# Kernel optimization log

Hardware: AMD Instinct MI355X
Metric: run time of the kernel (lower is better)

Reference implementation:

```python
import jax, jax.numpy as jnp
import numpy as np

B, N, D = 2, 2048, 1024
H = 16                      # num_heads, head_dim = 64
E, K, CF = 4, 2, 1.0        # num_experts, top_k, capacity_factor
MLP_H = int(D * 4.0)        # dense Mlp hidden (mlp_ratio=4.0)
MOE_H = int(D * 0.25)       # expert hidden (hard-coded dim*0.25 in source)


def setup_inputs() -> dict:
    key = jax.random.key(0)
    ks = jax.random.split(key, 12)
    r = lambda k, shp, s=0.02: jax.random.normal(k, shp, jnp.float32) * s
    return dict(
        x=jax.random.normal(ks[0], (B, N, D), jnp.float32),
        noise=jax.random.normal(ks[1], (B, N, E), jnp.float32),
        ln1_g=jnp.ones((D,), jnp.float32), ln1_b=jnp.zeros((D,), jnp.float32),
        ln2_g=jnp.ones((D,), jnp.float32), ln2_b=jnp.zeros((D,), jnp.float32),
        w_qkv=r(ks[2], (3 * D, D)),
        w_proj=r(ks[3], (D, D)), b_proj=jnp.zeros((D,), jnp.float32),
        w_route=r(ks[4], (D, E), 0.05), b_route=jnp.zeros((E,), jnp.float32),
        w_noise=r(ks[5], (D, E), 0.05), b_noise=jnp.zeros((E,), jnp.float32),
        we1=r(ks[6], (E, D, MOE_H)), be1=jnp.zeros((E, MOE_H), jnp.float32),
        we2=r(ks[7], (E, MOE_H, D)), be2=jnp.zeros((E, D), jnp.float32),
        w_mlp1=r(ks[8], (D, MLP_H)), b_mlp1=jnp.zeros((MLP_H,), jnp.float32),
        w_mlp2=r(ks[9], (MLP_H, D)), b_mlp2=jnp.zeros((D,), jnp.float32),
    )


def _ln(x, g, b, eps=1e-5):
    mu = x.mean(-1, keepdims=True)
    var = ((x - mu) ** 2).mean(-1, keepdims=True)
    return (x - mu) * jax.lax.rsqrt(var + eps) * g + b


def _gelu(x):
    return jax.nn.gelu(x, approximate=False)  # torch nn.GELU default (erf)


def reference(x, noise, ln1_g, ln1_b, ln2_g, ln2_b, w_qkv, w_proj, b_proj,
              w_route, b_route, w_noise, b_noise, we1, be1, we2, be2,
              w_mlp1, b_mlp1, w_mlp2, b_mlp2):
    Bs, Ns, Ds = x.shape
    hd = Ds // H
    # --- attention branch ---
    x1 = _ln(x, ln1_g, ln1_b)
    qkv = (x1 @ w_qkv.T).reshape(Bs, Ns, 3, H, hd).transpose(2, 0, 3, 1, 4)
    q, k, v = qkv[0] * (hd ** -0.5), qkv[1], qkv[2]
    attn = jax.nn.softmax(jnp.einsum('bhnd,bhmd->bhnm', q, k), axis=-1)
    ao = jnp.einsum('bhnm,bhmd->bhnd', attn, v).transpose(0, 2, 1, 3).reshape(Bs, Ns, Ds)
    x = x + (ao @ w_proj.T + b_proj)
    # --- shared norm for mlp + moe ---
    x2 = _ln(x, ln2_g, ln2_b)
    # --- noisy top-k router ---
    logits = x2 @ w_route + b_route                  # [B,N,E]
    noisy = logits + noise * jax.nn.softplus(x2 @ w_noise + b_noise)
    topv, topi = jax.lax.top_k(noisy, K)             # [B,N,K]
    probs = jax.nn.softmax(topv, axis=-1)            # softmax over sparse logits == softmax over top-k
    T = Bs * Ns
    flat_x = x2.reshape(T, Ds)
    fidx = topi.reshape(T, K)
    rows = jnp.arange(T)[:, None]
    gate = jnp.zeros((T, E), noisy.dtype).at[rows, fidx].set(probs.reshape(T, K))
    capacity = int(T * K / E * CF)
    # --- capacity-limited dispatch / expert MLP / combine ---
    def dispatch(eid, W1, b1, W2, b2):
        mask = jnp.any(fidx == eid, axis=-1)                     # [T]
        order = jnp.argsort(jnp.logical_not(mask))               # stable: selected tokens first, in token order
        sel = order[:capacity]                                   # [C]
        valid = mask[sel].astype(flat_x.dtype)
        h = _gelu(flat_x[sel] @ W1 + b1)
        out = h @ W2 + b2
        w = gate[sel, eid] * valid
        return sel, out * w[:, None]
    sel, outw = jax.vmap(dispatch)(jnp.arange(E), we1, be1, we2, be2)   # [E,C], [E,C,D]
    moe = jnp.zeros_like(flat_x).at[sel.reshape(-1)].add(outw.reshape(-1, Ds)).reshape(Bs, Ns, Ds)
    # --- dense mlp branch ---
    mlp = _gelu(x2 @ w_mlp1 + b_mlp1) @ w_mlp2 + b_mlp2
    return x + mlp + moe
```

## Files before the change

### kernel.cpp

```cpp
#include <hip/hip_runtime.h>
#include <hip/hip_bf16.h>
#include <math.h>

typedef __bf16 bf16;
typedef __bf16 bf16x4 __attribute__((ext_vector_type(4)));
typedef __bf16 bf16x8 __attribute__((ext_vector_type(8)));
typedef float  f32x4  __attribute__((ext_vector_type(4)));

#define T_TOK 4096
#define DIM   1024
#define NHEAD 16
#define SEQ   2048
#define NEXP  4
#define CAP   2048
#define MLPH  4096
#define MOEH  256

__device__ __forceinline__ float gelu_exact(float v) {
    return 0.5f * v * (1.f + erff(v * 0.70710678118654752f));
}

struct HL { bf16 h, l; };
__device__ __forceinline__ HL split2(float v) {
    HL r; r.h = (bf16)v; r.l = (bf16)(v - (float)r.h); return r;
}

__device__ __forceinline__ float fast_exp2(float x) {
#if __has_builtin(__builtin_amdgcn_exp2f)
    return __builtin_amdgcn_exp2f(x);
#else
    return exp2f(x);
#endif
}

__device__ __forceinline__ void gload16(const bf16* gptr, bf16* lptr) {
    __builtin_amdgcn_global_load_lds(
        (const __attribute__((address_space(1))) unsigned int*)gptr,
        (__attribute__((address_space(3))) unsigned int*)lptr,
        16, 0, 0);
}

__device__ __forceinline__ bf16x8 sw_frag(const bf16* arr, int row, int cc) {
    return *(const bf16x8*)&arr[row * 64 + ((cc ^ (row & 7)) * 8)];
}

__device__ __forceinline__ void xcd_tile(int& bx, int& by) {
    int gx = gridDim.x;
    int nwg = gx * gridDim.y;
    int flat = blockIdx.y * gx + blockIdx.x;
    int q = nwg >> 3, r = nwg & 7;
    int xcd = flat & 7, loc = flat >> 3;
    int swz = (xcd < r ? xcd * (q + 1) : r * (q + 1) + (xcd - r) * q) + loc;
    bx = swz % gx; by = swz / gx;
}

__global__ __launch_bounds__(256)
void ln_split_kernel(const float* __restrict__ x, const float* __restrict__ g,
                     const float* __restrict__ b, bf16* __restrict__ oh, bf16* __restrict__ ol) {
    int wave = threadIdx.x >> 6, lane = threadIdx.x & 63;
    long t = (long)blockIdx.x * 4 + wave;
    const float* xr = x + t * DIM;
    float v[16];
    #pragma unroll
    for (int i = 0; i < 16; i++) v[i] = xr[i * 64 + lane];
    float s = 0.f, s2 = 0.f;
    #pragma unroll
    for (int i = 0; i < 16; i++) { s += v[i]; s2 += v[i] * v[i]; }
    #pragma unroll
    for (int m = 1; m < 64; m <<= 1) { s += __shfl_xor(s, m); s2 += __shfl_xor(s2, m); }
    float mu  = s * (1.f / DIM);
    float var = s2 * (1.f / DIM) - mu * mu;
    float rs  = 1.f / sqrtf(var + 1e-5f);
    #pragma unroll
    for (int i = 0; i < 16; i++) {
        int d = i * 64 + lane;
        HL sp = split2((v[i] - mu) * rs * g[d] + b[d]);
        oh[t * DIM + d] = sp.h; ol[t * DIM + d] = sp.l;
    }
}

__global__ __launch_bounds__(256)
void split_pair_kernel(const float* __restrict__ in, bf16* __restrict__ h, bf16* __restrict__ l) {
    long i0 = ((long)blockIdx.x * 256 + threadIdx.x) * 4;
    f32x4 v = *(const f32x4*)&in[i0];
    bf16x4 vh, vl;
    #pragma unroll
    for (int j = 0; j < 4; j++) { HL sp = split2(v[j]); vh[j] = sp.h; vl[j] = sp.l; }
    *(bf16x4*)&h[i0] = vh; *(bf16x4*)&l[i0] = vl;
}

__global__ __launch_bounds__(256)
void transpose_conv_kernel(const float* __restrict__ in, bf16* __restrict__ out, int R, int C) {
    __shared__ bf16 tile[32][33];
    long bo = (long)blockIdx.z * R * C;
    in += bo; out += bo;
    int c0 = blockIdx.x * 32, r0 = blockIdx.y * 32;
    int tx = threadIdx.x & 31, ty = threadIdx.x >> 5;
    #pragma unroll
    for (int i = 0; i < 32; i += 8)
        tile[ty + i][tx] = (bf16)in[(long)(r0 + ty + i) * C + c0 + tx];
    __syncthreads();
    #pragma unroll
    for (int i = 0; i < 32; i += 8)
        out[(long)(c0 + ty + i) * R + r0 + tx] = tile[tx][ty + i];
}

__global__ __launch_bounds__(256)
void gemm_qkv(const bf16* __restrict__ Ah_g, const bf16* __restrict__ Al_g,
              const bf16* __restrict__ Bh_g, const bf16* __restrict__ Bl_g,
              bf16* __restrict__ Qh_g, bf16* __restrict__ Ql_g,
              bf16* __restrict__ Kh_g, bf16* __restrict__ Kl_g,
              bf16* __restrict__ VtI) {
    const int K = DIM;
    __shared__ alignas(16) bf16 Ah[8192], Al[8192], Bh[8192], Bl[8192];
    int tid = threadIdx.x;
    int wave = tid >> 6, lane = tid & 63;
    int l16 = lane & 15, l4 = lane >> 4;
    int wr = (wave >> 1) * 64, wc = (wave & 1) * 64;
    int bx, by; xcd_tile(bx, by);
    int row0 = by * 128, col0 = bx * 128;
    int r8s = lane >> 3;
    int colb = ((lane & 7) ^ r8s) * 8;
    f32x4 acc[4][4] = {};
    for (int k0 = 0; k0 < K; k0 += 64) {
        #pragma unroll
        for (int p = 0; p < 4; p++) {
            int rl = p * 32 + wave * 8 + r8s;
            int lb = p * 2048 + wave * 512;
            gload16(&Ah_g[(long)(row0 + rl) * K + k0 + colb], &Ah[lb]);
            gload16(&Al_g[(long)(row0 + rl) * K + k0 + colb], &Al[lb]);
            gload16(&Bh_g[(long)(col0 + rl) * K + k0 + colb], &Bh[lb]);
            gload16(&Bl_g[(long)(col0 + rl) * K + k0 + colb], &Bl[lb]);
        }
        __syncthreads();
        #pragma unroll
        for (int ks = 0; ks < 2; ks++) {
            bf16x8 ah[4], al[4], bh[4], bl[4];
            #pragma unroll
            for (int i = 0; i < 4; i++) {
                ah[i] = sw_frag(Ah, wr + i*16 + l16, ks*4 + l4);
                al[i] = sw_frag(Al, wr + i*16 + l16, ks*4 + l4);
            }
            #pragma unroll
            for (int j = 0; j < 4; j++) {
                bh[j] = sw_frag(Bh, wc + j*16 + l16, ks*4 + l4);
                bl[j] = sw_frag(Bl, wc + j*16 + l16, ks*4 + l4);
            }
            #pragma unroll
            for (int i = 0; i < 4; i++)
                #pragma unroll
                for (int j = 0; j < 4; j++) {
                    acc[i][j] = __builtin_amdgcn_mfma_f32_16x16x32_bf16(ah[i], bh[j], acc[i][j], 0, 0, 0);
                    acc[i][j] = __builtin_amdgcn_mfma_f32_16x16x32_bf16(ah[i], bl[j], acc[i][j], 0, 0, 0);
                    acc[i][j] = __builtin_amdgcn_mfma_f32_16x16x32_bf16(al[i], bh[j], acc[i][j], 0, 0, 0);
                }
        }
        __syncthreads();
    }
    if (col0 < 2048) {
        bool isQ = (col0 < 1024);
        bf16* oh = isQ ? Qh_g : Kh_g;
        bf16* ol = isQ ? Ql_g : Kl_g;
        float qscale = isQ ? 0.18033688011112043f : 1.0f;
        #pragma unroll
        for (int i = 0; i < 4; i++)
            #pragma unroll
            for (int r = 0; r < 4; r++) {
                int t = row0 + wr + i * 16 + l4 * 4 + r;
                int bq = t >> 11, s = t & 2047;
                #pragma unroll
                for (int j = 0; j < 4; j++) {
                    int col = (col0 + wc + j * 16 + l16) & 1023;
                    int hh = col >> 6, dl = col & 63;
                    long o = ((long)(bq * NHEAD + hh) * SEQ + s) * 64 + dl;
                    HL sp = split2(acc[i][j][r] * qscale);
                    oh[o] = sp.h;
                    if (!isQ) ol[o] = sp.l;
                }
            }
    } else {
        #pragma unroll
        for (int i = 0; i < 4; i++) {
            int s0 = row0 + wr + i * 16 + l4 * 4;
            int b = s0 >> 11, sl = s0 & 2047;
            #pragma unroll
            for (int j = 0; j < 4; j++) {
                int d = col0 - 2048 + wc + j * 16 + l16;
                int h = d >> 6, dl = d & 63;
                long base = ((long)(b * NHEAD + h) * 64 + dl) * (2 * SEQ) + 2 * sl;
                bf16x8 vi;
                #pragma unroll
                for (int r = 0; r < 4; r++) {
                    HL sp = split2(acc[i][j][r]);
                    vi[2 * r] = sp.h; vi[2 * r + 1] = sp.l;
                }
                *(bf16x8*)&VtI[base] = vi;
            }
        }
    }
}

__global__ __launch_bounds__(512, 4)
void flash_attn(const bf16* __restrict__ Qh_g,
                const bf16* __restrict__ Kh_g, const bf16* __restrict__ Kl_g,
                const bf16* __restrict__ VtI_g,
                bf16* __restrict__ aoh, bf16* __restrict__ aol) {
    __shared__ alignas(16) bf16 KhS[2][4096], KlS[2][4096], VIS[2][8192];
    int tid = threadIdx.x;
    int wave = tid >> 6, lane = tid & 63;
    int l16 = lane & 15, l4 = lane >> 4;
    int bid = blockIdx.x;
    int bh = bid & 31;
    int b = bh >> 4, h = bh & 15;
    int q0 = (bid >> 5) * 128;

    bf16x8 qfh[2];
    {
        const bf16* qh = Qh_g + ((long)bh * SEQ + q0 + wave * 16 + l16) * 64;
        #pragma unroll
        for (int ks = 0; ks < 2; ks++)
            qfh[ks] = *(const bf16x8*)&qh[ks * 32 + l4 * 8];
    }
    int r8 = lane >> 3;
    int c8 = lane & 7;
    int r4 = lane >> 4, c16 = lane & 15;
    const bf16* kh_g = Kh_g + (long)bh * SEQ * 64;
    const bf16* kl_g = Kl_g + (long)bh * SEQ * 64;
    const bf16* vI_g = VtI_g + (long)bh * 64 * (2 * SEQ);

    float m_s = -1e30f, l_s = 0.f;
    f32x4 accO[4] = {};

    auto stage = [&](int c0, int bsel) {
        int R0 = wave * 8;
        int row = R0 + r8;
        int ksw = (c8 ^ r8) * 8;
        gload16(&kh_g[(long)(c0 + row) * 64 + ksw], &KhS[bsel][R0 * 64]);
        gload16(&kl_g[(long)(c0 + row) * 64 + ksw], &KlS[bsel][R0 * 64]);
        #pragma unroll
        for (int q = 0; q < 2; q++) {
            int d0 = R0 + q * 4 + r4;
            gload16(&vI_g[(long)d0 * (2 * SEQ) + 2 * c0 + ((c16 ^ (d0 & 15)) * 8)],
                    &VIS[bsel][(R0 + q * 4) * 128]);
        }
    };

    auto compute = [&](const bf16* KhT, const bf16* KlT, const bf16* VIT) {
        f32x4 st[4] = {};
        __builtin_amdgcn_s_setprio(1);
        #pragma unroll
        for (int ks = 0; ks < 2; ks++) {
            #pragma unroll
            for (int i = 0; i < 4; i++) {
                bf16x8 akh = sw_frag(KhT, i * 16 + l16, ks * 4 + l4);
                bf16x8 akl = sw_frag(KlT, i * 16 + l16, ks * 4 + l4);
                st[i] = __builtin_amdgcn_mfma_f32_16x16x32_bf16(akh, qfh[ks], st[i], 0, 0, 0);
                st[i] = __builtin_amdgcn_mfma_f32_16x16x32_bf16(akl, qfh[ks], st[i], 0, 0, 0);
            }
        }
        __builtin_amdgcn_s_setprio(0);
        float mx = st[0][0];
        #pragma unroll
        for (int i = 0; i < 4; i++)
            #pragma unroll
            for (int r = 0; r < 4; r++) mx = fmaxf(mx, st[i][r]);
        mx = fmaxf(mx, __shfl_xor(mx, 16));
        mx = fmaxf(mx, __shfl_xor(mx, 32));
        if (!__all(mx <= m_s + 8.f)) {
            float mnew = fmaxf(m_s, mx);
            float alpha = fast_exp2(m_s - mnew);
            l_s *= alpha;
            #pragma unroll
            for (int i = 0; i < 4; i++)
                #pragma unroll
                for (int r = 0; r < 4; r++) accO[i][r] *= alpha;
            m_s = mnew;
        }
        float psum = 0.f;
        bf16x8 pw[4];
        #pragma unroll
        for (int kb = 0; kb < 4; kb++)
            #pragma unroll
            for (int r = 0; r < 4; r++) {
                float pv = fast_exp2(st[kb][r] - m_s);
                psum += pv;
                bf16 pb = (bf16)pv;
                pw[kb][2 * r] = pb; pw[kb][2 * r + 1] = pb;
            }
        psum += __shfl_xor(psum, 16);
        psum += __shfl_xor(psum, 32);
        l_s += psum;
        __builtin_amdgcn_s_setprio(1);
        #pragma unroll
        for (int kb = 0; kb < 4; kb++) {
            #pragma unroll
            for (int i = 0; i < 4; i++) {
                int d = i * 16 + l16;
                bf16x8 av = *(const bf16x8*)&VIT[d * 128 + (((kb * 4 + l4) ^ (d & 15)) * 8)];
                accO[i] = __builtin_amdgcn_mfma_f32_16x16x32_bf16(av, pw[kb], accO[i], 0, 0, 0);
            }
        }
        __builtin_amdgcn_s_setprio(0);
    };

    const int NT = SEQ / 64;
    stage(0, 0);
    #pragma unroll 1
    for (int t = 0; t < NT; t += 2) {
        stage((t + 1) * 64, 1);
        asm volatile("s_waitcnt vmcnt(4)" ::: "memory");
        __builtin_amdgcn_sched_barrier(0);
        __builtin_amdgcn_s_barrier();
        compute(KhS[0], KlS[0], VIS[0]);
        asm volatile("" ::: "memory");
        __builtin_amdgcn_s_barrier();
        if (t + 2 < NT) {
            stage((t + 2) * 64, 0);
            asm volatile("s_waitcnt vmcnt(4)" ::: "memory");
        } else {
            asm volatile("s_waitcnt vmcnt(0)" ::: "memory");
        }
        __builtin_amdgcn_sched_barrier(0);
        __builtin_amdgcn_s_barrier();
        compute(KhS[1], KlS[1], VIS[1]);
        asm volatile("" ::: "memory");
        __builtin_amdgcn_s_barrier();
    }

    float inv = 1.f / l_s;
    int q = q0 + wave * 16 + l16;
    #pragma unroll
    for (int i = 0; i < 4; i++) {
        bf16x4 oh4, ol4;
        #pragma unroll
        for (int r = 0; r < 4; r++) { HL sp = split2(accO[i][r] * inv); oh4[r] = sp.h; ol4[r] = sp.l; }
        long o = ((long)(b * SEQ + q)) * DIM + h * 64 + i * 16 + l4 * 4;
        *(bf16x4*)&aoh[o] = oh4;
        *(bf16x4*)&aol[o] = ol4;
    }
}

__global__ __launch_bounds__(256)
void gemm_proj(const bf16* __restrict__ Ah_g, const bf16* __restrict__ Al_g,
               const bf16* __restrict__ Bh_g, const bf16* __restrict__ Bl_g,
               const float* __restrict__ bias, const float* __restrict__ res,
               float* __restrict__ C, int N, int K) {
    __shared__ alignas(16) bf16 Ah[8192], Al[8192], Bh[8192], Bl[8192];
    int tid = threadIdx.x;
    int wave = tid >> 6, lane = tid & 63;
    int l16 = lane & 15, l4 = lane >> 4;
    int wr = (wave >> 1) * 64, wc = (wave & 1) * 64;
    int bx, by; xcd_tile(bx, by);
    int row0 = by * 128, col0 = bx * 128;
    int r8s = lane >> 3;
    int colb = ((lane & 7) ^ r8s) * 8;
    f32x4 acc[4][4] = {};
    for (int k0 = 0; k0 < K; k0 += 64) {
        #pragma unroll
        for (int p = 0; p < 4; p++) {
            int rl = p * 32 + wave * 8 + r8s;
            int lb = p * 2048 + wave * 512;
            gload16(&Ah_g[(long)(row0 + rl) * K + k0 + colb], &Ah[lb]);
            gload16(&Al_g[(long)(row0 + rl) * K + k0 + colb], &Al[lb]);
            gload16(&Bh_g[(long)(col0 + rl) * K + k0 + colb], &Bh[lb]);
            gload16(&Bl_g[(long)(col0 + rl) * K + k0 + colb], &Bl[lb]);
        }
        __syncthreads();
        #pragma unroll
        for (int ks = 0; ks < 2; ks++) {
            bf16x8 ah[4], al[4], bh[4], bl[4];
            #pragma unroll
            for (int i = 0; i < 4; i++) {
                ah[i] = sw_frag(Ah, wr + i*16 + l16, ks*4 + l4);
                al[i] = sw_frag(Al, wr + i*16 + l16, ks*4 + l4);
            }
            #pragma unroll
            for (int j = 0; j < 4; j++) {
                bh[j] = sw_frag(Bh, wc + j*16 + l16, ks*4 + l4);
                bl[j] = sw_frag(Bl, wc + j*16 + l16, ks*4 + l4);
            }
            #pragma unroll
            for (int i = 0; i < 4; i++)
                #pragma unroll
                for (int j = 0; j < 4; j++) {
                    acc[i][j] = __builtin_amdgcn_mfma_f32_16x16x32_bf16(ah[i], bh[j], acc[i][j], 0, 0, 0);
                    acc[i][j] = __builtin_amdgcn_mfma_f32_16x16x32_bf16(ah[i], bl[j], acc[i][j], 0, 0, 0);
                    acc[i][j] = __builtin_amdgcn_mfma_f32_16x16x32_bf16(al[i], bh[j], acc[i][j], 0, 0, 0);
                }
        }
        __syncthreads();
    }
    #pragma unroll
    for (int i = 0; i < 4; i++)
        #pragma unroll
        for (int r = 0; r < 4; r++) {
            int grow = row0 + wr + i * 16 + l4 * 4 + r;
            #pragma unroll
            for (int j = 0; j < 4; j++) {
                int gcol = col0 + wc + j * 16 + l16;
                long o = (long)grow * N + gcol;
                C[o] = acc[i][j][r] + bias[gcol] + res[o];
            }
        }
}

template<bool BIAS, bool GELU, bool GATHER, int OUT_MODE>
__global__ __launch_bounds__(256)
void gemm_bt(const bf16* __restrict__ A, const bf16* __restrict__ Bt,
             const float* __restrict__ bias,
             bf16* __restrict__ Cbf, float* __restrict__ Cf,
             const int* __restrict__ rowmap, const float* __restrict__ roww,
             int M, int N, int K,
             long eA, long eB, long ebias, long eMap, long eC) {
    int ez = blockIdx.z;
    A += (long)ez * eA; Bt += (long)ez * eB;
    if (BIAS) bias += (long)ez * ebias;
    if (GATHER || OUT_MODE == 3) rowmap += (long)ez * eMap;
    if (OUT_MODE == 3) roww += (long)ez * eMap;
    if (OUT_MODE == 0) Cbf += (long)ez * eC;

    __shared__ alignas(16) bf16 As[8192];
    __shared__ alignas(16) bf16 Bs[8192];
    int tid = threadIdx.x;
    int wave = tid >> 6, lane = tid & 63;
    int l16 = lane & 15, l4 = lane >> 4;
    int wr = (wave >> 1) * 64, wc = (wave & 1) * 64;
    int bx, by; xcd_tile(bx, by);
    int row0 = by * 128, col0 = bx * 128;
    int r8s = lane >> 3;
    int colb = ((lane & 7) ^ r8s) * 8;

    long arow[4];
    #pragma unroll
    for (int p = 0; p < 4; p++) {
        long gr = row0 + p * 32 + wave * 8 + r8s;
        if (GATHER) gr = rowmap[gr];
        arow[p] = gr;
    }
    f32x4 acc[4][4] = {};
    for (int k0 = 0; k0 < K; k0 += 64) {
        #pragma unroll
        for (int p = 0; p < 4; p++) {
            int rl = p * 32 + wave * 8 + r8s;
            int lb = p * 2048 + wave * 512;
            gload16(&A[arow[p] * K + k0 + colb], &As[lb]);
            gload16(&Bt[(long)(col0 + rl) * K + k0 + colb], &Bs[lb]);
        }
        __syncthreads();
        #pragma unroll
        for (int ks = 0; ks < 2; ks++) {
            bf16x8 af[4], bfr[4];
            #pragma unroll
            for (int i = 0; i < 4; i++) af[i]  = sw_frag(As, wr + i*16 + l16, ks*4 + l4);
            #pragma unroll
            for (int j = 0; j < 4; j++) bfr[j] = sw_frag(Bs, wc + j*16 + l16, ks*4 + l4);
            #pragma unroll
            for (int i = 0; i < 4; i++)
                #pragma unroll
                for (int j = 0; j < 4; j++)
                    acc[i][j] = __builtin_amdgcn_mfma_f32_16x16x32_bf16(af[i], bfr[j], acc[i][j], 0, 0, 0);
        }
        __syncthreads();
    }
    #pragma unroll
    for (int i = 0; i < 4; i++)
        #pragma unroll
        for (int r = 0; r < 4; r++) {
            int grow = row0 + wr + i * 16 + l4 * 4 + r;
            int st = 0; float sw = 0.f;
            if (OUT_MODE == 3) { st = rowmap[grow]; sw = roww[grow]; }
            #pragma unroll
            for (int j = 0; j < 4; j++) {
                int gcol = col0 + wc + j * 16 + l16;
                float v = acc[i][j][r];
                if (BIAS) v += bias[gcol];
                if (GELU) v = gelu_exact(v);
                if (OUT_MODE == 0) {
                    Cbf[(long)grow * N + gcol] = (bf16)v;
                } else if (OUT_MODE == 2) {
                    long o = (long)grow * N + gcol;
                    Cf[o] += v;
                } else {
                    atomicAdd(&Cf[(long)st * N + gcol], sw * v);
                }
            }
        }
}

__global__ __launch_bounds__(256)
void routing_kernel(const float* __restrict__ xres, const float* __restrict__ g,
                    const float* __restrict__ b, const float* __restrict__ w_route,
                    const float* __restrict__ b_route, const float* __restrict__ w_noise,
                    const float* __restrict__ b_noise, const float* __restrict__ noise,
                    int* __restrict__ topi, float* __restrict__ topp,
                    bf16* __restrict__ x2b) {
    int wave = threadIdx.x >> 6, lane = threadIdx.x & 63;
    long t = (long)blockIdx.x * 4 + wave;
    const float* xr = xres + t * DIM;
    float v[16];
    #pragma unroll
    for (int i = 0; i < 16; i++) v[i] = xr[i * 64 + lane];
    float s = 0.f, s2 = 0.f;
    #pragma unroll
    for (int i = 0; i < 16; i++) { s += v[i]; s2 += v[i] * v[i]; }
    #pragma unroll
    for (int m = 1; m < 64; m <<= 1) { s += __shfl_xor(s, m); s2 += __shfl_xor(s2, m); }
    float mu  = s * (1.f / DIM);
    float var = s2 * (1.f / DIM) - mu * mu;
    float rs  = 1.f / sqrtf(var + 1e-5f);
    float accr[4] = {0.f,0.f,0.f,0.f}, accn[4] = {0.f,0.f,0.f,0.f};
    #pragma unroll
    for (int i = 0; i < 16; i++) {
        int d = i * 64 + lane;
        float n = (v[i] - mu) * rs * g[d] + b[d];
        x2b[t * DIM + d] = (bf16)n;
        #pragma unroll
        for (int e = 0; e < 4; e++) {
            accr[e] += n * w_route[d * 4 + e];
            accn[e] += n * w_noise[d * 4 + e];
        }
    }
    #pragma unroll
    for (int e = 0; e < 4; e++)
        #pragma unroll
        for (int m = 1; m < 64; m <<= 1) {
            accr[e] += __shfl_xor(accr[e], m);
            accn[e] += __shfl_xor(accn[e], m);
        }
    if (lane == 0) {
        float nz[4];
        #pragma unroll
        for (int e = 0; e < 4; e++) {
            float logit = accr[e] + b_route[e];
            float si = accn[e] + b_noise[e];
            float sp = si > 0.f ? si + log1pf(expf(-si)) : log1pf(expf(si));
            nz[e] = logit + noise[t * 4 + e] * sp;
        }
        int i1 = 0;
        #pragma unroll
        for (int e = 1; e < 4; e++) if (nz[e] > nz[i1]) i1 = e;
        int i2 = -1; float v2 = -1e30f;
        #pragma unroll
        for (int e = 0; e < 4; e++) if (e != i1 && nz[e] > v2) { v2 = nz[e]; i2 = e; }
        float ex = expf(v2 - nz[i1]);
        topi[t * 2]     = i1; topi[t * 2 + 1] = i2;
        topp[t * 2]     = 1.f / (1.f + ex);
        topp[t * 2 + 1] = ex / (1.f + ex);
    }
}

__global__ __launch_bounds__(256)
void dispatch_kernel(const int* __restrict__ topi, const float* __restrict__ topp,
                     int* __restrict__ sel, float* __restrict__ wgt) {
    int e = threadIdx.x >> 6, lane = threadIdx.x & 63;
    int cnt = 0;
    for (int c = 0; c < T_TOK; c += 64) {
        int t = c + lane;
        int i0 = topi[t * 2], i1 = topi[t * 2 + 1];
        bool m = (i0 == e) || (i1 == e);
        unsigned long long bal = __ballot(m);
        int pos = cnt + __popcll(bal & ((1ull << lane) - 1ull));
        if (m && pos < CAP) {
            sel[e * CAP + pos] = t;
            wgt[e * CAP + pos] = (i0 == e) ? topp[t * 2] : topp[t * 2 + 1];
        }
        cnt += (int)__popcll(bal);
    }
    if (cnt > CAP) cnt = CAP;
    for (int pos = cnt + lane; pos < CAP; pos += 64) {
        sel[e * CAP + pos] = 0;
        wgt[e * CAP + pos] = 0.f;
    }
}

extern "C" void kernel_launch(void* const* d_in, const int* in_sizes, int n_in,
                              void* d_out, int out_size, void* d_ws, size_t ws_size,
                              hipStream_t stream) {
    (void)in_sizes; (void)n_in; (void)out_size; (void)ws_size;
    const float* x       = (const float*)d_in[0];
    const float* noise   = (const float*)d_in[1];
    const float* ln1_g   = (const float*)d_in[2];
    const float* ln1_b   = (const float*)d_in[3];
    const float* ln2_g   = (const float*)d_in[4];
    const float* ln2_b   = (const float*)d_in[5];
    const float* w_qkv   = (const float*)d_in[6];
    const float* w_proj  = (const float*)d_in[7];
    const float* b_proj  = (const float*)d_in[8];
    const float* w_route = (const float*)d_in[9];
    const float* b_route = (const float*)d_in[10];
    const float* w_noise = (const float*)d_in[11];
    const float* b_noise = (const float*)d_in[12];
    const float* we1     = (const float*)d_in[13];
    const float* be1     = (const float*)d_in[14];
    const float* we2     = (const float*)d_in[15];
    const float* be2     = (const float*)d_in[16];
    const float* w_mlp1  = (const float*)d_in[17];
    const float* b_mlp1  = (const float*)d_in[18];
    const float* w_mlp2  = (const float*)d_in[19];
    const float* b_mlp2  = (const float*)d_in[20];
    float* d_outf = (float*)d_out;

    const size_t MB = 1024 * 1024;
    char* ws = (char*)d_ws;
    bf16* x1h = (bf16*)(ws);
    bf16* x1l = (bf16*)(ws + 8 * MB);
    bf16* aoh = (bf16*)(ws);
    bf16* aol = (bf16*)(ws + 8 * MB);
    bf16* w_mlp1T = (bf16*)(ws);
    bf16* w_mlp2T = (bf16*)(ws + 8 * MB);
    bf16* wqkvh = (bf16*)(ws + 16 * MB);
    bf16* wqkvl = (bf16*)(ws + 22 * MB);
    bf16* we1T  = (bf16*)(ws + 16 * MB);
    bf16* we2T  = (bf16*)(ws + 18 * MB);
    bf16* h_e   = (bf16*)(ws + 20 * MB);
    bf16* wprojh = (bf16*)(ws + 28 * MB);
    bf16* wprojl = (bf16*)(ws + 30 * MB);
    bf16* Qh = (bf16*)(ws + 32 * MB);
    bf16* Ql = (bf16*)(ws + 40 * MB);
    bf16* Kh = (bf16*)(ws + 48 * MB);
    bf16* Kl = (bf16*)(ws + 56 * MB);
    bf16* h_mlp = (bf16*)(ws + 32 * MB);
    bf16*  VtI  = (bf16*)(ws + 64 * MB);
    bf16*  x2b  = (bf16*)(ws + 64 * MB);
    int*   topi = (int*)(ws + 72 * MB);
    float* topp = (float*)(ws + 72 * MB + 32768);
    int*   sel  = (int*)(ws + 72 * MB + 65536);
    float* wgt  = (float*)(ws + 72 * MB + 98304);

    ln_split_kernel<<<T_TOK/4, 256, 0, stream>>>(x, ln1_g, ln1_b, x1h, x1l);
    split_pair_kernel<<<(3*DIM*DIM)/1024, 256, 0, stream>>>(w_qkv, wqkvh, wqkvl);
    split_pair_kernel<<<(DIM*DIM)/1024,   256, 0, stream>>>(w_proj, wprojh, wprojl);

    gemm_qkv<<<dim3(3*DIM/128, T_TOK/128), 256, 0, stream>>>(
        x1h, x1l, wqkvh, wqkvl, Qh, Ql, Kh, Kl, VtI);

    flash_attn<<<dim3(32 * (SEQ/128)), 512, 0, stream>>>(Qh, Kh, Kl, VtI, aoh, aol);

    gemm_proj<<<dim3(DIM/128, T_TOK/128), 256, 0, stream>>>(
        aoh, aol, wprojh, wprojl, b_proj, x, d_outf, DIM, DIM);

    routing_kernel<<<T_TOK/4, 256, 0, stream>>>(d_outf, ln2_g, ln2_b, w_route, b_route,
                                                w_noise, b_noise, noise, topi, topp, x2b);
    dispatch_kernel<<<1, 256, 0, stream>>>(topi, topp, sel, wgt);

    transpose_conv_kernel<<<dim3(MLPH/32, DIM/32, 1),    256, 0, stream>>>(w_mlp1, w_mlp1T, DIM, MLPH);
    transpose_conv_kernel<<<dim3(DIM/32, MLPH/32, 1),    256, 0, stream>>>(w_mlp2, w_mlp2T, MLPH, DIM);
    transpose_conv_kernel<<<dim3(MOEH/32, DIM/32, NEXP), 256, 0, stream>>>(we1, we1T, DIM, MOEH);
    transpose_conv_kernel<<<dim3(DIM/32, MOEH/32, NEXP), 256, 0, stream>>>(we2, we2T, MOEH, DIM);

    gemm_bt<true,true,false,0><<<dim3(MLPH/128, T_TOK/128), 256, 0, stream>>>(
        x2b, w_mlp1T, b_mlp1, h_mlp, nullptr, nullptr, nullptr, T_TOK, MLPH, DIM,
        0, 0, 0, 0, 0);
    gemm_bt<true,false,false,2><<<dim3(DIM/128, T_TOK/128), 256, 0, stream>>>(
        h_mlp, w_mlp2T, b_mlp2, nullptr, d_outf, nullptr, nullptr, T_TOK, DIM, MLPH,
        0, 0, 0, 0, 0);

    gemm_bt<true,true,true,0><<<dim3(MOEH/128, CAP/128, NEXP), 256, 0, stream>>>(
        x2b, we1T, be1, h_e, nullptr, sel, nullptr, CAP, MOEH, DIM,
        0, (long)MOEH*DIM, MOEH, CAP, (long)CAP*MOEH);
    gemm_bt<true,false,false,3><<<dim3(DIM/128, CAP/128, NEXP), 256, 0, stream>>>(
        h_e, we2T, be2, nullptr, d_outf, sel, wgt, CAP, DIM, MOEH,
        (long)CAP*MOEH, (long)DIM*MOEH, DIM, CAP, 0);
}
```

Measured before the change: 626.4 us.

## Double-buffer GEMM LDS tiles with BK=32 and overlap global loads with MFMA

The three GEMM kernels now use a two-stage LDS ping-pong with K-tile 32, issuing the next tile's global_load_lds before computing the current one. Explicit vmcnt waits, raw s_barrier and setprio around the MFMA bursts replace the old load-then-sync loop, with a new 32-wide swizzle. The qkv/proj kernels also drop the XCD tile remap, and the two weight-split launches are merged into one. This aims to hide global memory latency behind MFMA work, but the hand-written waitcnt counts must match the load count per stage, and losing the XCD swizzle may reduce L2 locality.

```diff
diff --git a/kernel.cpp b/kernel.cpp
--- a/kernel.cpp
+++ b/kernel.cpp
@@ -43,6 +43,9 @@
 __device__ __forceinline__ bf16x8 sw_frag(const bf16* arr, int row, int cc) {
     return *(const bf16x8*)&arr[row * 64 + ((cc ^ (row & 7)) * 8)];
 }
+__device__ __forceinline__ bf16x8 sw32(const bf16* arr, int row, int c) {
+    return *(const bf16x8*)&arr[row * 32 + ((c ^ ((row >> 1) & 3)) * 8)];
+}
 
 __device__ __forceinline__ void xcd_tile(int& bx, int& by) {
     int gx = gridDim.x;
@@ -80,13 +83,18 @@
 }
 
 __global__ __launch_bounds__(256)
-void split_pair_kernel(const float* __restrict__ in, bf16* __restrict__ h, bf16* __restrict__ l) {
+void split_pair2_kernel(const float* __restrict__ in1, bf16* __restrict__ h1, bf16* __restrict__ l1,
+                        long n1,
+                        const float* __restrict__ in2, bf16* __restrict__ h2, bf16* __restrict__ l2) {
     long i0 = ((long)blockIdx.x * 256 + threadIdx.x) * 4;
-    f32x4 v = *(const f32x4*)&in[i0];
+    const float* in; bf16 *h, *l;
+    if (i0 < n1) { in = in1 + i0; h = h1 + i0; l = l1 + i0; }
+    else         { long j = i0 - n1; in = in2 + j; h = h2 + j; l = l2 + j; }
+    f32x4 v = *(const f32x4*)in;
     bf16x4 vh, vl;
     #pragma unroll
     for (int j = 0; j < 4; j++) { HL sp = split2(v[j]); vh[j] = sp.h; vl[j] = sp.l; }
-    *(bf16x4*)&h[i0] = vh; *(bf16x4*)&l[i0] = vl;
+    *(bf16x4*)h = vh; *(bf16x4*)l = vl;
 }
 
 __global__ __launch_bounds__(256)
@@ -112,51 +120,72 @@
               bf16* __restrict__ Kh_g, bf16* __restrict__ Kl_g,
               bf16* __restrict__ VtI) {
     const int K = DIM;
-    __shared__ alignas(16) bf16 Ah[8192], Al[8192], Bh[8192], Bl[8192];
+    __shared__ alignas(16) bf16 AhS[2][4096], AlS[2][4096], BhS[2][4096], BlS[2][4096];
     int tid = threadIdx.x;
     int wave = tid >> 6, lane = tid & 63;
     int l16 = lane & 15, l4 = lane >> 4;
     int wr = (wave >> 1) * 64, wc = (wave & 1) * 64;
-    int bx, by; xcd_tile(bx, by);
-    int row0 = by * 128, col0 = bx * 128;
-    int r8s = lane >> 3;
-    int colb = ((lane & 7) ^ r8s) * 8;
+    int row0 = blockIdx.y * 128, col0 = blockIdx.x * 128;
+    int sr = lane >> 2, ss = lane & 3;
+    int csrc = (ss ^ ((sr >> 1) & 3)) * 8;
     f32x4 acc[4][4] = {};
-    for (int k0 = 0; k0 < K; k0 += 64) {
-        #pragma unroll
-        for (int p = 0; p < 4; p++) {
-            int rl = p * 32 + wave * 8 + r8s;
-            int lb = p * 2048 + wave * 512;
-            gload16(&Ah_g[(long)(row0 + rl) * K + k0 + colb], &Ah[lb]);
-            gload16(&Al_g[(long)(row0 + rl) * K + k0 + colb], &Al[lb]);
-            gload16(&Bh_g[(long)(col0 + rl) * K + k0 + colb], &Bh[lb]);
-            gload16(&Bl_g[(long)(col0 + rl) * K + k0 + colb], &Bl[lb]);
-        }
-        __syncthreads();
-        #pragma unroll
-        for (int ks = 0; ks < 2; ks++) {
-            bf16x8 ah[4], al[4], bh[4], bl[4];
-            #pragma unroll
-            for (int i = 0; i < 4; i++) {
-                ah[i] = sw_frag(Ah, wr + i*16 + l16, ks*4 + l4);
-                al[i] = sw_frag(Al, wr + i*16 + l16, ks*4 + l4);
-            }
+
+    auto stage = [&](int k0, int bsel) {
+        #pragma unroll
+        for (int p = 0; p < 2; p++) {
+            int ri = (p * 4 + wave) * 16 + sr;
+            int lb = (p * 4 + wave) * 512;
+            gload16(&Ah_g[(long)(row0 + ri) * K + k0 + csrc], &AhS[bsel][lb]);
+            gload16(&Al_g[(long)(row0 + ri) * K + k0 + csrc], &AlS[bsel][lb]);
+            gload16(&Bh_g[(long)(col0 + ri) * K + k0 + csrc], &BhS[bsel][lb]);
+            gload16(&Bl_g[(long)(col0 + ri) * K + k0 + csrc], &BlS[bsel][lb]);
+        }
+    };
+    auto compute = [&](const bf16* Ah_, const bf16* Al_, const bf16* Bh_, const bf16* Bl_) {
+        bf16x8 ah[4], al[4], bh[4], bl[4];
+        #pragma unroll
+        for (int i = 0; i < 4; i++) {
+            ah[i] = sw32(Ah_, wr + i * 16 + l16, l4);
+            al[i] = sw32(Al_, wr + i * 16 + l16, l4);
+            bh[i] = sw32(Bh_, wc + i * 16 + l16, l4);
+            bl[i] = sw32(Bl_, wc + i * 16 + l16, l4);
+        }
+        __builtin_amdgcn_s_setprio(1);
+        #pragma unroll
+        for (int i = 0; i < 4; i++)
             #pragma unroll
             for (int j = 0; j < 4; j++) {
-                bh[j] = sw_frag(Bh, wc + j*16 + l16, ks*4 + l4);
-                bl[j] = sw_frag(Bl, wc + j*16 + l16, ks*4 + l4);
-            }
-            #pragma unroll
-            for (int i = 0; i < 4; i++)
-                #pragma unroll
-                for (int j = 0; j < 4; j++) {
-                    acc[i][j] = __builtin_amdgcn_mfma_f32_16x16x32_bf16(ah[i], bh[j], acc[i][j], 0, 0, 0);
-                    acc[i][j] = __builtin_amdgcn_mfma_f32_16x16x32_bf16(ah[i], bl[j], acc[i][j], 0, 0, 0);
-                    acc[i][j] = __builtin_amdgcn_mfma_f32_16x16x32_bf16(al[i], bh[j], acc[i][j], 0, 0, 0);
-                }
-        }
-        __syncthreads();
-    }
+                acc[i][j] = __builtin_amdgcn_mfma_f32_16x16x32_bf16(ah[i], bh[j], acc[i][j], 0, 0, 0);
+                acc[i][j] = __builtin_amdgcn_mfma_f32_16x16x32_bf16(ah[i], bl[j], acc[i][j], 0, 0, 0);
+                acc[i][j] = __builtin_amdgcn_mfma_f32_16x16x32_bf16(al[i], bh[j], acc[i][j], 0, 0, 0);
+            }
+        __builtin_amdgcn_s_setprio(0);
+    };
+
+    const int NT = K / 32;
+    stage(0, 0);
+    #pragma unroll 1
+    for (int t = 0; t < NT; t += 2) {
+        stage((t + 1) * 32, 1);
+        asm volatile("s_waitcnt vmcnt(8)" ::: "memory");
+        __builtin_amdgcn_sched_barrier(0);
+        __builtin_amdgcn_s_barrier();
+        compute(AhS[0], AlS[0], BhS[0], BlS[0]);
+        asm volatile("" ::: "memory");
+        __builtin_amdgcn_s_barrier();
+        if (t + 2 < NT) {
+            stage((t + 2) * 32, 0);
+            asm volatile("s_waitcnt vmcnt(8)" ::: "memory");
+        } else {
+            asm volatile("s_waitcnt vmcnt(0)" ::: "memory");
+        }
+        __builtin_amdgcn_sched_barrier(0);
+        __builtin_amdgcn_s_barrier();
+        compute(AhS[1], AlS[1], BhS[1], BlS[1]);
+        asm volatile("" ::: "memory");
+        __builtin_amdgcn_s_barrier();
+    }
+
     if (col0 < 2048) {
         bool isQ = (col0 < 1024);
         bf16* oh = isQ ? Qh_g : Kh_g;
@@ -345,51 +374,72 @@
                const bf16* __restrict__ Bh_g, const bf16* __restrict__ Bl_g,
                const float* __restrict__ bias, const float* __restrict__ res,
                float* __restrict__ C, int N, int K) {
-    __shared__ alignas(16) bf16 Ah[8192], Al[8192], Bh[8192], Bl[8192];
+    __shared__ alignas(16) bf16 AhS[2][4096], AlS[2][4096], BhS[2][4096], BlS[2][4096];
     int tid = threadIdx.x;
     int wave = tid >> 6, lane = tid & 63;
     int l16 = lane & 15, l4 = lane >> 4;
     int wr = (wave >> 1) * 64, wc = (wave & 1) * 64;
-    int bx, by; xcd_tile(bx, by);
-    int row0 = by * 128, col0 = bx * 128;
-    int r8s = lane >> 3;
-    int colb = ((lane & 7) ^ r8s) * 8;
+    int row0 = blockIdx.y * 128, col0 = blockIdx.x * 128;
+    int sr = lane >> 2, ss = lane & 3;
+    int csrc = (ss ^ ((sr >> 1) & 3)) * 8;
     f32x4 acc[4][4] = {};
-    for (int k0 = 0; k0 < K; k0 += 64) {
-        #pragma unroll
-        for (int p = 0; p < 4; p++) {
-            int rl = p * 32 + wave * 8 + r8s;
-            int lb = p * 2048 + wave * 512;
-            gload16(&Ah_g[(long)(row0 + rl) * K + k0 + colb], &Ah[lb]);
-            gload16(&Al_g[(long)(row0 + rl) * K + k0 + colb], &Al[lb]);
-            gload16(&Bh_g[(long)(col0 + rl) * K + k0 + colb], &Bh[lb]);
-            gload16(&Bl_g[(long)(col0 + rl) * K + k0 + colb], &Bl[lb]);
-        }
-        __syncthreads();
-        #pragma unroll
-        for (int ks = 0; ks < 2; ks++) {
-            bf16x8 ah[4], al[4], bh[4], bl[4];
-            #pragma unroll
-            for (int i = 0; i < 4; i++) {
-                ah[i] = sw_frag(Ah, wr + i*16 + l16, ks*4 + l4);
-                al[i] = sw_frag(Al, wr + i*16 + l16, ks*4 + l4);
-            }
+
+    auto stage = [&](int k0, int bsel) {
+        #pragma unroll
+        for (int p = 0; p < 2; p++) {
+            int ri = (p * 4 + wave) * 16 + sr;
+            int lb = (p * 4 + wave) * 512;
+            gload16(&Ah_g[(long)(row0 + ri) * K + k0 + csrc], &AhS[bsel][lb]);
+            gload16(&Al_g[(long)(row0 + ri) * K + k0 + csrc], &AlS[bsel][lb]);
+            gload16(&Bh_g[(long)(col0 + ri) * K + k0 + csrc], &BhS[bsel][lb]);
+            gload16(&Bl_g[(long)(col0 + ri) * K + k0 + csrc], &BlS[bsel][lb]);
+        }
+    };
+    auto compute = [&](const bf16* Ah_, const bf16* Al_, const bf16* Bh_, const bf16* Bl_) {
+        bf16x8 ah[4], al[4], bh[4], bl[4];
+        #pragma unroll
+        for (int i = 0; i < 4; i++) {
+            ah[i] = sw32(Ah_, wr + i * 16 + l16, l4);
+            al[i] = sw32(Al_, wr + i * 16 + l16, l4);
+            bh[i] = sw32(Bh_, wc + i * 16 + l16, l4);
+            bl[i] = sw32(Bl_, wc + i * 16 + l16, l4);
+        }
+        __builtin_amdgcn_s_setprio(1);
+        #pragma unroll
+        for (int i = 0; i < 4; i++)
             #pragma unroll
             for (int j = 0; j < 4; j++) {
-                bh[j] = sw_frag(Bh, wc + j*16 + l16, ks*4 + l4);
-                bl[j] = sw_frag(Bl, wc + j*16 + l16, ks*4 + l4);
-            }
-            #pragma unroll
-            for (int i = 0; i < 4; i++)
-                #pragma unroll
-                for (int j = 0; j < 4; j++) {
-                    acc[i][j] = __builtin_amdgcn_mfma_f32_16x16x32_bf16(ah[i], bh[j], acc[i][j], 0, 0, 0);
-                    acc[i][j] = __builtin_amdgcn_mfma_f32_16x16x32_bf16(ah[i], bl[j], acc[i][j], 0, 0, 0);
-                    acc[i][j] = __builtin_amdgcn_mfma_f32_16x16x32_bf16(al[i], bh[j], acc[i][j], 0, 0, 0);
-                }
-        }
-        __syncthreads();
-    }
+                acc[i][j] = __builtin_amdgcn_mfma_f32_16x16x32_bf16(ah[i], bh[j], acc[i][j], 0, 0, 0);
+                acc[i][j] = __builtin_amdgcn_mfma_f32_16x16x32_bf16(ah[i], bl[j], acc[i][j], 0, 0, 0);
+                acc[i][j] = __builtin_amdgcn_mfma_f32_16x16x32_bf16(al[i], bh[j], acc[i][j], 0, 0, 0);
+            }
+        __builtin_amdgcn_s_setprio(0);
+    };
+
+    const int NT = K / 32;
+    stage(0, 0);
+    #pragma unroll 1
+    for (int t = 0; t < NT; t += 2) {
+        stage((t + 1) * 32, 1);
+        asm volatile("s_waitcnt vmcnt(8)" ::: "memory");
+        __builtin_amdgcn_sched_barrier(0);
+        __builtin_amdgcn_s_barrier();
+        compute(AhS[0], AlS[0], BhS[0], BlS[0]);
+        asm volatile("" ::: "memory");
+        __builtin_amdgcn_s_barrier();
+        if (t + 2 < NT) {
+            stage((t + 2) * 32, 0);
+            asm volatile("s_waitcnt vmcnt(8)" ::: "memory");
+        } else {
+            asm volatile("s_waitcnt vmcnt(0)" ::: "memory");
+        }
+        __builtin_amdgcn_sched_barrier(0);
+        __builtin_amdgcn_s_barrier();
+        compute(AhS[1], AlS[1], BhS[1], BlS[1]);
+        asm volatile("" ::: "memory");
+        __builtin_amdgcn_s_barrier();
+    }
+
     #pragma unroll
     for (int i = 0; i < 4; i++)
         #pragma unroll
@@ -419,49 +469,75 @@
     if (OUT_MODE == 3) roww += (long)ez * eMap;
     if (OUT_MODE == 0) Cbf += (long)ez * eC;
 
-    __shared__ alignas(16) bf16 As[8192];
-    __shared__ alignas(16) bf16 Bs[8192];
+    __shared__ alignas(16) bf16 AsS[2][4096], BsS[2][4096];
     int tid = threadIdx.x;
     int wave = tid >> 6, lane = tid & 63;
     int l16 = lane & 15, l4 = lane >> 4;
     int wr = (wave >> 1) * 64, wc = (wave & 1) * 64;
     int bx, by; xcd_tile(bx, by);
     int row0 = by * 128, col0 = bx * 128;
-    int r8s = lane >> 3;
-    int colb = ((lane & 7) ^ r8s) * 8;
-
-    long arow[4];
-    #pragma unroll
-    for (int p = 0; p < 4; p++) {
-        long gr = row0 + p * 32 + wave * 8 + r8s;
+    int sr = lane >> 2, ss = lane & 3;
+    int csrc = (ss ^ ((sr >> 1) & 3)) * 8;
+
+    long arow2[2]; int bri[2];
+    #pragma unroll
+    for (int p = 0; p < 2; p++) {
+        int ri = (p * 4 + wave) * 16 + sr;
+        long gr = row0 + ri;
         if (GATHER) gr = rowmap[gr];
-        arow[p] = gr;
+        arow2[p] = gr;
+        bri[p] = col0 + ri;
     }
     f32x4 acc[4][4] = {};
-    for (int k0 = 0; k0 < K; k0 += 64) {
-        #pragma unroll
-        for (int p = 0; p < 4; p++) {
-            int rl = p * 32 + wave * 8 + r8s;
-            int lb = p * 2048 + wave * 512;
-            gload16(&A[arow[p] * K + k0 + colb], &As[lb]);
-            gload16(&Bt[(long)(col0 + rl) * K + k0 + colb], &Bs[lb]);
-        }
-        __syncthreads();
-        #pragma unroll
-        for (int ks = 0; ks < 2; ks++) {
-            bf16x8 af[4], bfr[4];
-            #pragma unroll
-            for (int i = 0; i < 4; i++) af[i]  = sw_frag(As, wr + i*16 + l16, ks*4 + l4);
-            #pragma unroll
-            for (int j = 0; j < 4; j++) bfr[j] = sw_frag(Bs, wc + j*16 + l16, ks*4 + l4);
-            #pragma unroll
-            for (int i = 0; i < 4; i++)
-                #pragma unroll
-                for (int j = 0; j < 4; j++)
-                    acc[i][j] = __builtin_amdgcn_mfma_f32_16x16x32_bf16(af[i], bfr[j], acc[i][j], 0, 0, 0);
-        }
-        __syncthreads();
-    }
+
+    auto stage = [&](int k0, int bsel) {
+        #pragma unroll
+        for (int p = 0; p < 2; p++) {
+            int lb = (p * 4 + wave) * 512;
+            gload16(&A[arow2[p] * K + k0 + csrc], &AsS[bsel][lb]);
+            gload16(&Bt[(long)bri[p] * K + k0 + csrc], &BsS[bsel][lb]);
+        }
+    };
+    auto compute = [&](const bf16* As_, const bf16* Bs_) {
+        bf16x8 af[4], bfr[4];
+        #pragma unroll
+        for (int i = 0; i < 4; i++) {
+            af[i]  = sw32(As_, wr + i * 16 + l16, l4);
+            bfr[i] = sw32(Bs_, wc + i * 16 + l16, l4);
+        }
+        __builtin_amdgcn_s_setprio(1);
+        #pragma unroll
+        for (int i = 0; i < 4; i++)
+            #pragma unroll
+            for (int j = 0; j < 4; j++)
+                acc[i][j] = __builtin_amdgcn_mfma_f32_16x16x32_bf16(af[i], bfr[j], acc[i][j], 0, 0, 0);
+        __builtin_amdgcn_s_setprio(0);
+    };
+
+    const int NT = K / 32;
+    stage(0, 0);
+    #pragma unroll 1
+    for (int t = 0; t < NT; t += 2) {
+        stage((t + 1) * 32, 1);
+        asm volatile("s_waitcnt vmcnt(4)" ::: "memory");
+        __builtin_amdgcn_sched_barrier(0);
+        __builtin_amdgcn_s_barrier();
+        compute(AsS[0], BsS[0]);
+        asm volatile("" ::: "memory");
+        __builtin_amdgcn_s_barrier();
+        if (t + 2 < NT) {
+            stage((t + 2) * 32, 0);
+            asm volatile("s_waitcnt vmcnt(4)" ::: "memory");
+        } else {
+            asm volatile("s_waitcnt vmcnt(0)" ::: "memory");
+        }
+        __builtin_amdgcn_sched_barrier(0);
+        __builtin_amdgcn_s_barrier();
+        compute(AsS[1], BsS[1]);
+        asm volatile("" ::: "memory");
+        __builtin_amdgcn_s_barrier();
+    }
+
     #pragma unroll
     for (int i = 0; i < 4; i++)
         #pragma unroll
@@ -628,8 +704,8 @@
     float* wgt  = (float*)(ws + 72 * MB + 98304);
 
     ln_split_kernel<<<T_TOK/4, 256, 0, stream>>>(x, ln1_g, ln1_b, x1h, x1l);
-    split_pair_kernel<<<(3*DIM*DIM)/1024, 256, 0, stream>>>(w_qkv, wqkvh, wqkvl);
-    split_pair_kernel<<<(DIM*DIM)/1024,   256, 0, stream>>>(w_proj, wprojh, wprojl);
+    split_pair2_kernel<<<(4*DIM*DIM)/1024, 256, 0, stream>>>(
+        w_qkv, wqkvh, wqkvl, (long)3*DIM*DIM, w_proj, wprojh, wprojl);
 
     gemm_qkv<<<dim3(3*DIM/128, T_TOK/128), 256, 0, stream>>>(
         x1h, x1l, wqkvh, wqkvl, Qh, Ql, Kh, Kl, VtI);
```

Result: no change. 624.9 us (-0.2%).
